# Performance work log

Hardware: AMD Instinct MI355X
Metric: run time of the kernel (lower is better)

## Reference

```python
import jax, jax.numpy as jnp
import numpy as np
import math

E, N, K, R = 1024, 16, 4, 64  # embed_dim, state_dim, d_conv, dt_rank=ceil(E/16)
B, L = 2, 2048


def setup_inputs() -> dict:
    key = jax.random.key(0)
    ks = jax.random.split(key, 8)
    gn = lambda k, sh, sc: jax.random.normal(k, sh, dtype=jnp.float32) * sc
    W_z = gn(ks[0], (E, E), E ** -0.5)                      # in_proj_z weight (no bias)
    W_params = gn(ks[1], (R + 2 * N, E), E ** -0.5)         # in_proj_params weight (no bias)
    conv_w = gn(ks[2], (E, 1, K), 0.5)                      # depthwise conv1d weight, no bias
    dt_std = R ** -0.5 * 0.1
    W_dt = jax.random.uniform(ks[3], (E, R), jnp.float32, -dt_std, dt_std)
    b_dt = jnp.full((E,), math.log(math.expm1(0.001)), dtype=jnp.float32)
    A_log = jnp.tile(jnp.log(jnp.arange(1, N + 1, dtype=jnp.float32))[None, :], (E, 1))
    D = jnp.ones((E,), dtype=jnp.float32)
    W_out = gn(ks[4], (E, E), E ** -0.5)
    x = jax.random.normal(ks[5], (B, L, E), dtype=jnp.float32)
    return dict(x=x, W_z=W_z, W_params=W_params, conv_w=conv_w, W_dt=W_dt,
                b_dt=b_dt, A_log=A_log, D=D, W_out=W_out)


def reference(x, W_z, W_params, conv_w, W_dt, b_dt, A_log, D, W_out):
    b, l, e = x.shape
    n = A_log.shape[1]
    r = W_dt.shape[1]
    k = conv_w.shape[-1]

    z = x @ W_z.T                                           # [B,L,E]
    params = x @ W_params.T                                 # [B,L,R+2N]
    dt_unproj = params[..., :r]
    # B_proj = params[..., r:r+n] is computed but UNUSED in the original forward
    C_proj = params[..., r + n:]                            # [B,L,N]
    dt = jax.nn.softplus(dt_unproj @ W_dt.T + b_dt)         # [B,L,E]

    # depthwise causal conv: torch pads K-1 both sides then slices [:L] == left-pad K-1
    xc = jax.lax.conv_general_dilated(
        x.transpose(0, 2, 1), conv_w, (1,), [(k - 1, 0)],
        dimension_numbers=('NCH', 'OIH', 'NCH'), feature_group_count=e)
    u = jax.nn.silu(xc.transpose(0, 2, 1))                  # [B,L,E]

    A = -jnp.exp(A_log)                                     # [E,N]
    A_tilde = jnp.exp(dt[..., None] * A[None, None])        # [B,L,E,N]
    B_tilde = jnp.where(jnp.abs(A)[None, None] < 1e-5,
                        dt[..., None],
                        (A_tilde - 1.0) / (A[None, None] + 1e-10))

    # recurrence (note t-1 indexing, faithful to original):
    # h_0 = B~[0]*u[0];  h_t = A~[t-1]*h_{t-1} + B~[t-1]*u[t-1]
    h0 = B_tilde[:, 0] * u[:, 0, :, None]                   # [B,E,N]

    def step(h, inp):
        a, bt, uu = inp
        h_new = a * h + bt * uu[..., None]
        return h_new, h_new

    xs = (A_tilde[:, :-1].transpose(1, 0, 2, 3),
          B_tilde[:, :-1].transpose(1, 0, 2, 3),
          u[:, :-1].transpose(1, 0, 2))
    _, hs = jax.lax.scan(step, h0, xs)                      # [L-1,B,E,N]
    h = jnp.concatenate([h0[None], hs], axis=0).transpose(1, 0, 2, 3)  # [B,L,E,N]

    y = jnp.einsum('bln,blen->ble', C_proj, h)
    y_ssm = y + u * D
    y_gated = y_ssm * jax.nn.silu(z)
    return y_gated @ W_out.T
```

## Files before the change

### kernel.cpp

```cpp
#include <hip/hip_runtime.h>
#include <math.h>

#define B_ 2
#define L_ 2048
#define E_ 1024
#define N_ 16
#define R_ 64
#define PWP 128
#define BL_ (B_*L_)

using bf16x8 = __attribute__((ext_vector_type(8))) short;
using f32x4  = __attribute__((ext_vector_type(4))) float;

__device__ __forceinline__ float softplusf(float x) {
    return fmaxf(x, 0.0f) + log1pf(expf(-fabsf(x)));
}
__device__ __forceinline__ float siluf(float x) {
    return x / (1.0f + expf(-x));
}
__device__ __forceinline__ ushort f2bf(float f) {
    unsigned u = __float_as_uint(f);
    return (ushort)((u + 0x7fffu + ((u >> 16) & 1u)) >> 16);
}
__device__ __forceinline__ float bf2f(ushort h) {
    return __uint_as_float(((unsigned)h) << 16);
}
__device__ __forceinline__ void gload16(const ushort* g, ushort* l) {
    __builtin_amdgcn_global_load_lds((const __attribute__((address_space(1))) void*)g,
                                     (__attribute__((address_space(3))) void*)l, 16, 0, 0);
}

__device__ __forceinline__ void split_body(const float* __restrict__ src, int spitch,
                                           int rows_src, ushort* __restrict__ dst,
                                           int K, int total4, int idx) {
    if (idx >= total4) return;
    const int Kq = K >> 2;
    const int r  = idx / Kq;
    const int c4 = (idx - r * Kq) << 2;
    float f[4] = {0.f, 0.f, 0.f, 0.f};
    if (r < rows_src)
        *reinterpret_cast<float4*>(f) = *reinterpret_cast<const float4*>(src + (size_t)r * spitch + c4);
    ushort h[4], lo[4];
#pragma unroll
    for (int q = 0; q < 4; ++q) {
        h[q]  = f2bf(f[q]);
        lo[q] = f2bf(f[q] - bf2f(h[q]));
    }
    ushort* d0 = dst + (size_t)r * 2 * K + c4;
    *reinterpret_cast<uint2*>(d0)     = make_uint2((uint)h[0]  | ((uint)h[1]  << 16), (uint)h[2]  | ((uint)h[3]  << 16));
    *reinterpret_cast<uint2*>(d0 + K) = make_uint2((uint)lo[0] | ((uint)lo[1] << 16), (uint)lo[2] | ((uint)lo[3] << 16));
}

__global__ __launch_bounds__(256)
void split_rm(const float* __restrict__ src, int spitch, int rows_src,
              ushort* __restrict__ dst, int K, int total4) {
    split_body(src, spitch, rows_src, dst, K, total4, blockIdx.x * 256 + threadIdx.x);
}

__global__ __launch_bounds__(256)
void split_w3(const float* __restrict__ Wz, const float* __restrict__ Wp,
              const float* __restrict__ Wdt, ushort* __restrict__ WzC,
              ushort* __restrict__ WpC, ushort* __restrict__ WdtC) {
    const int idx = blockIdx.x * 256 + threadIdx.x;
    if (blockIdx.y == 0)      split_body(Wz,  E_, E_,  WzC,  E_, E_ * E_ / 4, idx);
    else if (blockIdx.y == 1) split_body(Wp,  E_, 96,  WpC,  E_, 128 * E_ / 4, idx);
    else                      split_body(Wdt, R_, E_,  WdtC, R_, E_ * R_ / 4, idx);
}

__global__ __launch_bounds__(256)
void split_tr(const float* __restrict__ ygT, ushort* __restrict__ Ycat) {
    __shared__ float Ts[64][65];
    const int e0 = blockIdx.x * 64;
    const int l0 = blockIdx.y * 64;
    const int b  = blockIdx.z;
    const int tid = threadIdx.x;
    for (int idx = tid; idx < 64 * 64; idx += 256) {
        const int rr = idx >> 6, cc = idx & 63;
        Ts[rr][cc] = ygT[((size_t)(b * E_ + e0 + rr) << 11) + l0 + cc];
    }
    __syncthreads();
    for (int idx = tid; idx < 64 * 16; idx += 256) {
        const int rl = idx >> 4, g = idx & 15;
        ushort h[4], lo[4];
#pragma unroll
        for (int q = 0; q < 4; ++q) {
            const float f = Ts[g * 4 + q][rl];
            h[q]  = f2bf(f);
            lo[q] = f2bf(f - bf2f(h[q]));
        }
        ushort* d0 = Ycat + (size_t)(b * L_ + l0 + rl) * 2 * E_ + e0 + g * 4;
        *reinterpret_cast<uint2*>(d0)      = make_uint2((uint)h[0]  | ((uint)h[1]  << 16), (uint)h[2]  | ((uint)h[3]  << 16));
        *reinterpret_cast<uint2*>(d0 + E_) = make_uint2((uint)lo[0] | ((uint)lo[1] << 16), (uint)lo[2] | ((uint)lo[3] << 16));
    }
}

template<int BM, int BN, int MODE>
__global__ __launch_bounds__(256)
void mfma_gemm(const ushort* __restrict__ A, const ushort* __restrict__ Bm,
               const float* __restrict__ bias, ushort* __restrict__ P2,
               float* __restrict__ C, int Kd, int Ncols) {
    constexpr int WTM = BM / 2, WTN = BN / 2;
    constexpr int MI = WTM / 16, NJ = WTN / 16;
    __shared__ ushort As[BM * 64];
    __shared__ ushort Bs[BN * 64];
    const int tid  = threadIdx.x;
    const int wave = tid >> 6, lane = tid & 63;
    const int m0 = blockIdx.x * BM, n0 = blockIdx.y * BN;
    const int wr = wave >> 1, wc = wave & 1;
    const int fr = lane & 15, fg = lane >> 4;
    const int kxor = (fr & 7) << 3;
    const int pK = 2 * Kd;
    const int K64 = Kd >> 6;

    f32x4 acc[MI][NJ];
#pragma unroll
    for (int i = 0; i < MI; ++i)
#pragma unroll
        for (int j = 0; j < NJ; ++j) { f32x4 z = {0.f, 0.f, 0.f, 0.f}; acc[i][j] = z; }

    const int lrow = lane >> 3;
    const int lc   = lane & 7;

    for (int seg = 0; seg < 3; ++seg) {
        const int ao = (seg == 2) ? Kd : 0;
        const int bo = (seg == 1) ? Kd : 0;
        for (int tt = 0; tt < K64; ++tt) {
            const int ka = ao + tt * 64, kb = bo + tt * 64;
#pragma unroll
            for (int g = 0; g < BM / 32; ++g) {
                const int srow = (wave * (BM / 32) + g) * 8 + lrow;
                gload16(A + (size_t)(m0 + srow) * pK + ka + ((lc ^ (srow & 7)) * 8),
                        As + srow * 64 + lc * 8);
            }
#pragma unroll
            for (int g = 0; g < BN / 32; ++g) {
                const int srow = (wave * (BN / 32) + g) * 8 + lrow;
                gload16(Bm + (size_t)(n0 + srow) * pK + kb + ((lc ^ (srow & 7)) * 8),
                        Bs + srow * 64 + lc * 8);
            }
            __syncthreads();

            bf16x8 av[2][MI], bv[2][NJ];
#pragma unroll
            for (int ks = 0; ks < 2; ++ks) {
#pragma unroll
                for (int i = 0; i < MI; ++i) {
                    const int row = wr * WTM + i * 16 + fr;
                    av[ks][i] = *reinterpret_cast<const bf16x8*>(&As[row * 64 + ((ks * 32 + fg * 8) ^ kxor)]);
                }
#pragma unroll
                for (int j = 0; j < NJ; ++j) {
                    const int row = wc * WTN + j * 16 + fr;
                    bv[ks][j] = *reinterpret_cast<const bf16x8*>(&Bs[row * 64 + ((ks * 32 + fg * 8) ^ kxor)]);
                }
            }
#pragma unroll
            for (int ks = 0; ks < 2; ++ks)
#pragma unroll
                for (int i = 0; i < MI; ++i)
#pragma unroll
                    for (int j = 0; j < NJ; ++j)
                        acc[i][j] = __builtin_amdgcn_mfma_f32_16x16x32_bf16(av[ks][i], bv[ks][j], acc[i][j], 0, 0, 0);
            __syncthreads();
        }
    }

    if constexpr (MODE == 0) {
#pragma unroll
        for (int i = 0; i < MI; ++i) {
            const int m = m0 + wr * WTM + i * 16 + fg * 4;
#pragma unroll
            for (int j = 0; j < NJ; ++j) {
                const int n = n0 + wc * WTN + j * 16 + fr;
#pragma unroll
                for (int r = 0; r < 4; ++r)
                    C[(size_t)(m + r) * Ncols + n] = acc[i][j][r];
            }
        }
    } else if constexpr (MODE == 3) {
#pragma unroll
        for (int i = 0; i < MI; ++i) {
            const int m = m0 + wr * WTM + i * 16 + fg * 4;
#pragma unroll
            for (int j = 0; j < NJ; ++j) {
                const int n = n0 + wc * WTN + j * 16 + fr;
#pragma unroll
                for (int r = 0; r < 4; ++r) {
                    const float v = acc[i][j][r];
                    const int mm = m + r;
                    if (n < 64) {
                        const ushort hh = f2bf(v);
                        P2[(size_t)mm * 128 + n]      = hh;
                        P2[(size_t)mm * 128 + 64 + n] = f2bf(v - bf2f(hh));
                    } else if (n >= 80 && n < 96) {
                        C[(size_t)mm * Ncols + n] = v;
                    }
                }
            }
        }
    } else {
        const int b  = n0 >> 11;
        const int lb = n0 - (b << 11);
#pragma unroll
        for (int i = 0; i < MI; ++i) {
            const int e = m0 + wr * WTM + i * 16 + fg * 4;
#pragma unroll
            for (int r = 0; r < 4; ++r) {
                const float bia = (MODE == 2) ? bias[e + r] : 0.0f;
                float* row = C + ((size_t)(b * E_ + e + r) << 11) + lb;
#pragma unroll
                for (int j = 0; j < NJ; ++j) {
                    float v = acc[i][j][r];
                    if constexpr (MODE == 2) v = softplusf(v + bia);
                    row[wc * WTN + j * 16 + fr] = v;
                }
            }
        }
    }
}

__global__ __launch_bounds__(256)
void conv_silu_kernel(const float* __restrict__ x, const float* __restrict__ cw,
                      float* __restrict__ uT) {
    __shared__ float Xt[67][65];
    const int e0 = blockIdx.x * 64;
    const int l0 = blockIdx.y * 64;
    const int b  = blockIdx.z;
    const int tid = threadIdx.x;
    for (int idx = tid; idx < 67 * 64; idx += 256) {
        const int row = idx >> 6, col = idx & 63;
        const int gl = l0 - 3 + row;
        Xt[row][col] = (gl >= 0) ? x[((size_t)b * L_ + gl) * E_ + e0 + col] : 0.0f;
    }
    __syncthreads();
    const int lL = tid & 63;
    const int w  = tid >> 6;
    for (int ee = w; ee < 64; ee += 4) {
        const int e = e0 + ee;
        const float w0 = cw[e*4+0], w1 = cw[e*4+1], w2 = cw[e*4+2], w3 = cw[e*4+3];
        const float v = w0*Xt[lL][ee] + w1*Xt[lL+1][ee] + w2*Xt[lL+2][ee] + w3*Xt[lL+3][ee];
        uT[((size_t)b * E_ + e) * L_ + l0 + lL] = siluf(v);
    }
}

__global__ __launch_bounds__(64)
void scan_kernel(const float* __restrict__ dtT, const float* __restrict__ uT,
                 const float* __restrict__ zT, const float* __restrict__ params,
                 const float* __restrict__ A_log, const float* __restrict__ Dp,
                 float* __restrict__ ygT) {
    __shared__ float sdt[64 * 33];
    __shared__ float su [64 * 33];
    const int c = blockIdx.x;
    const int b = c >> 10;
    const int e = c & (E_ - 1);
    const int lane = threadIdx.x;
    constexpr int CH = L_ / 64;
    constexpr float LOG2E = 1.44269504088896340736f;

    const float* dtp = dtT + ((size_t)b * E_ + e) * L_;
    const float* up  = uT  + ((size_t)b * E_ + e) * L_;
    const float* zp  = zT  + ((size_t)b * E_ + e) * L_;

#pragma unroll
    for (int it = 0; it < 8; ++it) {
        const int l = (it * 64 + lane) * 4;
        const int slot = ((l >> 5) * 33) + (l & 31);
        float4 vd = *reinterpret_cast<const float4*>(dtp + l);
        float4 vu = *reinterpret_cast<const float4*>(up  + l);
        sdt[slot] = vd.x; sdt[slot+1] = vd.y; sdt[slot+2] = vd.z; sdt[slot+3] = vd.w;
        su [slot] = vu.x; su [slot+1] = vu.y; su [slot+2] = vu.z; su [slot+3] = vu.w;
    }

    float An2[N_], m1[N_], m2[N_], m3[N_];
#pragma unroll
    for (int n = 0; n < N_; ++n) {
        const float A = -expf(A_log[e * N_ + n]);
        An2[n] = A * LOG2E;
        const bool sel = fabsf(A) < 1e-5f;
        const float rA = 1.0f / (A + 1e-10f);
        m1[n] = sel ? 0.0f : rA;
        m2[n] = sel ? 1.0f : 0.0f;
        m3[n] = sel ? 0.0f : -rA;
    }
    const float Dv = Dp[e];
    __syncthreads();

    const int base = lane * 33;

    float P[N_], h[N_];
#pragma unroll
    for (int n = 0; n < N_; ++n) { P[n] = 1.0f; h[n] = 0.0f; }
#pragma unroll 4
    for (int j = 0; j < CH; ++j) {
        const float d  = sdt[base + j];
        const float uu = su [base + j];
#pragma unroll
        for (int n = 0; n < N_; ++n) {
            const float at = __builtin_amdgcn_exp2f(d * An2[n]);
            const float bt = fmaf(at, m1[n], fmaf(d, m2[n], m3[n]));
            h[n] = fmaf(at, h[n], bt * uu);
            P[n] *= at;
        }
    }

#pragma unroll
    for (int off = 1; off < 64; off <<= 1) {
#pragma unroll
        for (int n = 0; n < N_; ++n) {
            const float Pp = __shfl_up(P[n], off);
            const float Lp = __shfl_up(h[n], off);
            if (lane >= off) {
                h[n] = fmaf(P[n], Lp, h[n]);
                P[n] *= Pp;
            }
        }
    }

    float cP[N_], cL[N_];
#pragma unroll
    for (int n = 0; n < N_; ++n) {
        cP[n] = __shfl_up(P[n], 1);
        cL[n] = __shfl_up(h[n], 1);
    }

    const float d0 = sdt[0];
    const float u0 = su[0];
#pragma unroll
    for (int n = 0; n < N_; ++n) {
        const float at0 = __builtin_amdgcn_exp2f(d0 * An2[n]);
        const float bt0 = fmaf(at0, m1[n], fmaf(d0, m2[n], m3[n]));
        const float g0 = bt0 * u0;
        h[n] = (lane == 0) ? g0 : fmaf(cP[n], g0, cL[n]);
    }

    const float* crow = params + (size_t)b * L_ * PWP + 80;
    const int l0 = lane * CH;
#pragma unroll 4
    for (int j = 0; j < CH; ++j) {
        const float d  = sdt[base + j];
        const float uu = su [base + j];
        const float zv = zp[l0 + j];
        float Cv[N_];
        const float4* Cp4 = reinterpret_cast<const float4*>(crow + (size_t)(l0 + j) * PWP);
#pragma unroll
        for (int t = 0; t < N_ / 4; ++t)
            *reinterpret_cast<float4*>(Cv + t * 4) = Cp4[t];
        float y = 0.0f;
#pragma unroll
        for (int n = 0; n < N_; ++n) y = fmaf(Cv[n], h[n], y);
        const float outv = (y + uu * Dv) * siluf(zv);
        if (j < CH - 1) {
#pragma unroll
            for (int n = 0; n < N_; ++n) {
                const float at = __builtin_amdgcn_exp2f(d * An2[n]);
                const float bt = fmaf(at, m1[n], fmaf(d, m2[n], m3[n]));
                h[n] = fmaf(at, h[n], bt * uu);
            }
        }
        sdt[base + j] = outv;
    }
    __syncthreads();

    float* yp = ygT + ((size_t)b * E_ + e) * L_;
#pragma unroll
    for (int it = 0; it < 8; ++it) {
        const int l = (it * 64 + lane) * 4;
        const int slot = ((l >> 5) * 33) + (l & 31);
        float4 o;
        o.x = sdt[slot]; o.y = sdt[slot+1]; o.z = sdt[slot+2]; o.w = sdt[slot+3];
        *reinterpret_cast<float4*>(yp + l) = o;
    }
}

extern "C" void kernel_launch(void* const* d_in, const int* in_sizes, int n_in,
                              void* d_out, int out_size, void* d_ws, size_t ws_size,
                              hipStream_t stream) {
    const float* x     = (const float*)d_in[0];
    const float* W_z   = (const float*)d_in[1];
    const float* W_p   = (const float*)d_in[2];
    const float* cw    = (const float*)d_in[3];
    const float* W_dt  = (const float*)d_in[4];
    const float* b_dt  = (const float*)d_in[5];
    const float* A_log = (const float*)d_in[6];
    const float* Dp    = (const float*)d_in[7];
    const float* W_out = (const float*)d_in[8];
    float* out = (float*)d_out;

    char* w = (char*)d_ws;
    ushort* Xcat   = (ushort*)(w);
    ushort* Wzcat  = (ushort*)(w + 16777216);
    ushort* Wpcat  = (ushort*)(w + 20971520);
    ushort* Wdtcat = (ushort*)(w + 21495808);
    ushort* Pcat   = (ushort*)(w + 21757952);
    float*  params = (float*)(w + 22806528);
    float*  zT     = (float*)(w + 24903680);
    float*  dtT    = (float*)(w + 41680896);
    float*  uT     = (float*)(w + 58458112);
    float*  ygT    = (float*)(w + 75235328);
    ushort* Ycat   = Xcat;
    ushort* Wocat  = Wzcat;

    split_rm<<<4096, 256, 0, stream>>>(x, E_, BL_, Xcat, E_, BL_ * E_ / 4);
    split_w3<<<dim3(1024, 3), 256, 0, stream>>>(W_z, W_p, W_dt, Wzcat, Wpcat, Wdtcat);
    mfma_gemm<128,64,1><<<dim3(E_ / 128, BL_ / 64), 256, 0, stream>>>(
        Wzcat, Xcat, nullptr, nullptr, zT, E_, 0);
    mfma_gemm<64,64,3><<<dim3(BL_ / 64, 2), 256, 0, stream>>>(
        Xcat, Wpcat, nullptr, Pcat, params, E_, PWP);
    mfma_gemm<128,64,2><<<dim3(E_ / 128, BL_ / 64), 256, 0, stream>>>(
        Wdtcat, Pcat, b_dt, nullptr, dtT, R_, 0);
    conv_silu_kernel<<<dim3(E_ / 64, L_ / 64, B_), 256, 0, stream>>>(x, cw, uT);
    scan_kernel<<<B_ * E_, 64, 0, stream>>>(dtT, uT, zT, params, A_log, Dp, ygT);
    split_tr<<<dim3(E_ / 64, L_ / 64, B_), 256, 0, stream>>>(ygT, Ycat);
    split_rm<<<1024, 256, 0, stream>>>(W_out, E_, E_, Wocat, E_, E_ * E_ / 4);
    mfma_gemm<128,64,0><<<dim3(BL_ / 128, E_ / 64), 256, 0, stream>>>(
        Ycat, Wocat, nullptr, nullptr, out, E_, E_);
}
```

Measured before the change: 300.7 us.

## Parallelize scan over four waves and add BK template parameter to GEMM

The scan kernel grows from one wavefront to four per (batch, channel), with shorter per-thread chunks and a cross-wave prefix combine through shared memory. z is staged in LDS instead of read from global memory, and the selection masks are simplified. Separately, the MFMA GEMM gains a K-tile template parameter, and the larger GEMMs now use 128-wide K tiles. This means fewer barriers per K but more LDS per block, which may lower occupancy.

```diff
diff --git a/kernel.cpp b/kernel.cpp
--- a/kernel.cpp
+++ b/kernel.cpp
@@ -94,15 +94,18 @@
     }
 }
 
-template<int BM, int BN, int MODE>
+template<int BM, int BN, int BK, int MODE>
 __global__ __launch_bounds__(256)
 void mfma_gemm(const ushort* __restrict__ A, const ushort* __restrict__ Bm,
                const float* __restrict__ bias, ushort* __restrict__ P2,
                float* __restrict__ C, int Kd, int Ncols) {
     constexpr int WTM = BM / 2, WTN = BN / 2;
     constexpr int MI = WTM / 16, NJ = WTN / 16;
-    __shared__ ushort As[BM * 64];
-    __shared__ ushort Bs[BN * 64];
+    constexpr int CPR = BK / 8;
+    constexpr int KS  = BK / 32;
+    constexpr int RPW = 64 / CPR;
+    __shared__ ushort As[BM * BK];
+    __shared__ ushort Bs[BN * BK];
     const int tid  = threadIdx.x;
     const int wave = tid >> 6, lane = tid & 63;
     const int m0 = blockIdx.x * BM, n0 = blockIdx.y * BN;
@@ -110,7 +113,6 @@
     const int fr = lane & 15, fg = lane >> 4;
     const int kxor = (fr & 7) << 3;
     const int pK = 2 * Kd;
-    const int K64 = Kd >> 6;
 
     f32x4 acc[MI][NJ];
 #pragma unroll
@@ -118,49 +120,48 @@
 #pragma unroll
         for (int j = 0; j < NJ; ++j) { f32x4 z = {0.f, 0.f, 0.f, 0.f}; acc[i][j] = z; }
 
-    const int lrow = lane >> 3;
-    const int lc   = lane & 7;
-
+    const int lrow = lane / CPR;
+    const int lc   = lane % CPR;
+
+    const int KP = Kd / BK;
     for (int seg = 0; seg < 3; ++seg) {
         const int ao = (seg == 2) ? Kd : 0;
         const int bo = (seg == 1) ? Kd : 0;
-        for (int tt = 0; tt < K64; ++tt) {
-            const int ka = ao + tt * 64, kb = bo + tt * 64;
-#pragma unroll
-            for (int g = 0; g < BM / 32; ++g) {
-                const int srow = (wave * (BM / 32) + g) * 8 + lrow;
-                gload16(A + (size_t)(m0 + srow) * pK + ka + ((lc ^ (srow & 7)) * 8),
-                        As + srow * 64 + lc * 8);
-            }
-#pragma unroll
-            for (int g = 0; g < BN / 32; ++g) {
-                const int srow = (wave * (BN / 32) + g) * 8 + lrow;
-                gload16(Bm + (size_t)(n0 + srow) * pK + kb + ((lc ^ (srow & 7)) * 8),
-                        Bs + srow * 64 + lc * 8);
+        for (int tt = 0; tt < KP; ++tt) {
+            const int ka = ao + tt * BK, kb = bo + tt * BK;
+#pragma unroll
+            for (int g = 0; g < BM / (4 * RPW); ++g) {
+                const int srow = (wave * (BM / (4 * RPW)) + g) * RPW + lrow;
+                const int sc = (lc & 8) | ((lc ^ (srow & 7)) & 7);
+                gload16(A + (size_t)(m0 + srow) * pK + ka + sc * 8, As + srow * BK + lc * 8);
+            }
+#pragma unroll
+            for (int g = 0; g < BN / (4 * RPW); ++g) {
+                const int srow = (wave * (BN / (4 * RPW)) + g) * RPW + lrow;
+                const int sc = (lc & 8) | ((lc ^ (srow & 7)) & 7);
+                gload16(Bm + (size_t)(n0 + srow) * pK + kb + sc * 8, Bs + srow * BK + lc * 8);
             }
             __syncthreads();
 
-            bf16x8 av[2][MI], bv[2][NJ];
-#pragma unroll
-            for (int ks = 0; ks < 2; ++ks) {
+#pragma unroll
+            for (int ks = 0; ks < KS; ++ks) {
+                bf16x8 av[MI], bv[NJ];
 #pragma unroll
                 for (int i = 0; i < MI; ++i) {
                     const int row = wr * WTM + i * 16 + fr;
-                    av[ks][i] = *reinterpret_cast<const bf16x8*>(&As[row * 64 + ((ks * 32 + fg * 8) ^ kxor)]);
+                    av[i] = *reinterpret_cast<const bf16x8*>(&As[row * BK + ((ks * 32 + fg * 8) ^ kxor)]);
                 }
 #pragma unroll
                 for (int j = 0; j < NJ; ++j) {
                     const int row = wc * WTN + j * 16 + fr;
-                    bv[ks][j] = *reinterpret_cast<const bf16x8*>(&Bs[row * 64 + ((ks * 32 + fg * 8) ^ kxor)]);
+                    bv[j] = *reinterpret_cast<const bf16x8*>(&Bs[row * BK + ((ks * 32 + fg * 8) ^ kxor)]);
                 }
-            }
-#pragma unroll
-            for (int ks = 0; ks < 2; ++ks)
 #pragma unroll
                 for (int i = 0; i < MI; ++i)
 #pragma unroll
                     for (int j = 0; j < NJ; ++j)
-                        acc[i][j] = __builtin_amdgcn_mfma_f32_16x16x32_bf16(av[ks][i], bv[ks][j], acc[i][j], 0, 0, 0);
+                        acc[i][j] = __builtin_amdgcn_mfma_f32_16x16x32_bf16(av[i], bv[j], acc[i][j], 0, 0, 0);
+            }
             __syncthreads();
         }
     }
@@ -243,18 +244,22 @@
     }
 }
 
-__global__ __launch_bounds__(64)
+__global__ __launch_bounds__(256)
 void scan_kernel(const float* __restrict__ dtT, const float* __restrict__ uT,
                  const float* __restrict__ zT, const float* __restrict__ params,
                  const float* __restrict__ A_log, const float* __restrict__ Dp,
                  float* __restrict__ ygT) {
     __shared__ float sdt[64 * 33];
     __shared__ float su [64 * 33];
+    __shared__ float sz [64 * 33];
+    __shared__ float wPs[4][N_];
+    __shared__ float wLs[4][N_];
     const int c = blockIdx.x;
     const int b = c >> 10;
     const int e = c & (E_ - 1);
-    const int lane = threadIdx.x;
-    constexpr int CH = L_ / 64;
+    const int tid  = threadIdx.x;
+    const int wave = tid >> 6, lane = tid & 63;
+    constexpr int CH = 8;
     constexpr float LOG2E = 1.44269504088896340736f;
 
     const float* dtp = dtT + ((size_t)b * E_ + e) * L_;
@@ -262,42 +267,44 @@
     const float* zp  = zT  + ((size_t)b * E_ + e) * L_;
 
 #pragma unroll
-    for (int it = 0; it < 8; ++it) {
-        const int l = (it * 64 + lane) * 4;
+    for (int it = 0; it < 2; ++it) {
+        const int l = (it * 256 + tid) * 4;
         const int slot = ((l >> 5) * 33) + (l & 31);
         float4 vd = *reinterpret_cast<const float4*>(dtp + l);
         float4 vu = *reinterpret_cast<const float4*>(up  + l);
+        float4 vz = *reinterpret_cast<const float4*>(zp  + l);
         sdt[slot] = vd.x; sdt[slot+1] = vd.y; sdt[slot+2] = vd.z; sdt[slot+3] = vd.w;
         su [slot] = vu.x; su [slot+1] = vu.y; su [slot+2] = vu.z; su [slot+3] = vu.w;
-    }
-
-    float An2[N_], m1[N_], m2[N_], m3[N_];
+        sz [slot] = vz.x; sz [slot+1] = vz.y; sz [slot+2] = vz.z; sz [slot+3] = vz.w;
+    }
+
+    float An2[N_], rA[N_];
+    unsigned selm = 0;
 #pragma unroll
     for (int n = 0; n < N_; ++n) {
         const float A = -expf(A_log[e * N_ + n]);
         An2[n] = A * LOG2E;
-        const bool sel = fabsf(A) < 1e-5f;
-        const float rA = 1.0f / (A + 1e-10f);
-        m1[n] = sel ? 0.0f : rA;
-        m2[n] = sel ? 1.0f : 0.0f;
-        m3[n] = sel ? 0.0f : -rA;
+        if (fabsf(A) < 1e-5f) selm |= (1u << n);
+        rA[n] = 1.0f / (A + 1e-10f);
     }
     const float Dv = Dp[e];
     __syncthreads();
 
-    const int base = lane * 33;
+    const int base = (tid >> 2) * 33 + (tid & 3) * 8;
+    const float d0 = sdt[0];
+    const float u0 = su[0];
 
     float P[N_], h[N_];
 #pragma unroll
     for (int n = 0; n < N_; ++n) { P[n] = 1.0f; h[n] = 0.0f; }
-#pragma unroll 4
+#pragma unroll
     for (int j = 0; j < CH; ++j) {
         const float d  = sdt[base + j];
         const float uu = su [base + j];
 #pragma unroll
         for (int n = 0; n < N_; ++n) {
             const float at = __builtin_amdgcn_exp2f(d * An2[n]);
-            const float bt = fmaf(at, m1[n], fmaf(d, m2[n], m3[n]));
+            const float bt = ((selm >> n) & 1u) ? d : (at - 1.0f) * rA[n];
             h[n] = fmaf(at, h[n], bt * uu);
             P[n] *= at;
         }
@@ -316,30 +323,47 @@
         }
     }
 
+    if (lane == 63) {
+#pragma unroll
+        for (int n = 0; n < N_; ++n) { wPs[wave][n] = P[n]; wLs[wave][n] = h[n]; }
+    }
     float cP[N_], cL[N_];
 #pragma unroll
     for (int n = 0; n < N_; ++n) {
         cP[n] = __shfl_up(P[n], 1);
         cL[n] = __shfl_up(h[n], 1);
     }
-
-    const float d0 = sdt[0];
-    const float u0 = su[0];
+    __syncthreads();
+
+    float EP[N_], EL[N_];
+#pragma unroll
+    for (int n = 0; n < N_; ++n) { EP[n] = 1.0f; EL[n] = 0.0f; }
+    for (int w2 = 0; w2 < wave; ++w2) {
+#pragma unroll
+        for (int n = 0; n < N_; ++n) {
+            EL[n] = fmaf(wPs[w2][n], EL[n], wLs[w2][n]);
+            EP[n] *= wPs[w2][n];
+        }
+    }
 #pragma unroll
     for (int n = 0; n < N_; ++n) {
+        const float pl = (lane == 0) ? 1.0f : cP[n];
+        const float ll = (lane == 0) ? 0.0f : cL[n];
+        const float fP = pl * EP[n];
+        const float fL = fmaf(pl, EL[n], ll);
         const float at0 = __builtin_amdgcn_exp2f(d0 * An2[n]);
-        const float bt0 = fmaf(at0, m1[n], fmaf(d0, m2[n], m3[n]));
-        const float g0 = bt0 * u0;
-        h[n] = (lane == 0) ? g0 : fmaf(cP[n], g0, cL[n]);
+        const float bt0 = ((selm >> n) & 1u) ? d0 : (at0 - 1.0f) * rA[n];
+        const float g0  = bt0 * u0;
+        h[n] = fmaf(fP, g0, fL);
     }
 
     const float* crow = params + (size_t)b * L_ * PWP + 80;
-    const int l0 = lane * CH;
-#pragma unroll 4
+    const int l0 = tid * CH;
+#pragma unroll
     for (int j = 0; j < CH; ++j) {
         const float d  = sdt[base + j];
         const float uu = su [base + j];
-        const float zv = zp[l0 + j];
+        const float zv = sz [base + j];
         float Cv[N_];
         const float4* Cp4 = reinterpret_cast<const float4*>(crow + (size_t)(l0 + j) * PWP);
 #pragma unroll
@@ -353,21 +377,21 @@
 #pragma unroll
             for (int n = 0; n < N_; ++n) {
                 const float at = __builtin_amdgcn_exp2f(d * An2[n]);
-                const float bt = fmaf(at, m1[n], fmaf(d, m2[n], m3[n]));
+                const float bt = ((selm >> n) & 1u) ? d : (at - 1.0f) * rA[n];
                 h[n] = fmaf(at, h[n], bt * uu);
             }
         }
-        sdt[base + j] = outv;
+        sz[base + j] = outv;
     }
     __syncthreads();
 
     float* yp = ygT + ((size_t)b * E_ + e) * L_;
 #pragma unroll
-    for (int it = 0; it < 8; ++it) {
-        const int l = (it * 64 + lane) * 4;
+    for (int it = 0; it < 2; ++it) {
+        const int l = (it * 256 + tid) * 4;
         const int slot = ((l >> 5) * 33) + (l & 31);
         float4 o;
-        o.x = sdt[slot]; o.y = sdt[slot+1]; o.z = sdt[slot+2]; o.w = sdt[slot+3];
+        o.x = sz[slot]; o.y = sz[slot+1]; o.z = sz[slot+2]; o.w = sz[slot+3];
         *reinterpret_cast<float4*>(yp + l) = o;
     }
 }
@@ -402,16 +426,16 @@
 
     split_rm<<<4096, 256, 0, stream>>>(x, E_, BL_, Xcat, E_, BL_ * E_ / 4);
     split_w3<<<dim3(1024, 3), 256, 0, stream>>>(W_z, W_p, W_dt, Wzcat, Wpcat, Wdtcat);
-    mfma_gemm<128,64,1><<<dim3(E_ / 128, BL_ / 64), 256, 0, stream>>>(
+    mfma_gemm<128,64,128,1><<<dim3(E_ / 128, BL_ / 64), 256, 0, stream>>>(
         Wzcat, Xcat, nullptr, nullptr, zT, E_, 0);
-    mfma_gemm<64,64,3><<<dim3(BL_ / 64, 2), 256, 0, stream>>>(
+    mfma_gemm<64,64,128,3><<<dim3(BL_ / 64, 2), 256, 0, stream>>>(
         Xcat, Wpcat, nullptr, Pcat, params, E_, PWP);
-    mfma_gemm<128,64,2><<<dim3(E_ / 128, BL_ / 64), 256, 0, stream>>>(
+    mfma_gemm<128,64,64,2><<<dim3(E_ / 128, BL_ / 64), 256, 0, stream>>>(
         Wdtcat, Pcat, b_dt, nullptr, dtT, R_, 0);
     conv_silu_kernel<<<dim3(E_ / 64, L_ / 64, B_), 256, 0, stream>>>(x, cw, uT);
-    scan_kernel<<<B_ * E_, 64, 0, stream>>>(dtT, uT, zT, params, A_log, Dp, ygT);
+    scan_kernel<<<B_ * E_, 256, 0, stream>>>(dtT, uT, zT, params, A_log, Dp, ygT);
     split_tr<<<dim3(E_ / 64, L_ / 64, B_), 256, 0, stream>>>(ygT, Ycat);
     split_rm<<<1024, 256, 0, stream>>>(W_out, E_, E_, Wocat, E_, E_ * E_ / 4);
-    mfma_gemm<128,64,0><<<dim3(BL_ / 128, E_ / 64), 256, 0, stream>>>(
+    mfma_gemm<128,64,128,0><<<dim3(BL_ / 128, E_ / 64), 256, 0, stream>>>(
         Ycat, Wocat, nullptr, nullptr, out, E_, E_);
 }
```

Result: faster. 291.6 us (-3.0%).
